# Kernel tuning notes

Measured on AMD Instinct MI355X. Metric: run time of the kernel, lower is better.

The kernel has to match this reference:

```python
import jax, jax.numpy as jnp
import numpy as np

N = 100000          # nodes
E = 1600000         # edges
F = 128             # raw node features
D = 16              # embedding_dim (per-head out channels)
H = 8               # heads
NEG_SLOPE = 0.2     # GATConv leaky_relu slope
EPS = 1e-16         # PyG softmax denominator eps


def _glorot(key, shape):
    fan_in, fan_out = shape[0], shape[-1]
    lim = np.sqrt(6.0 / (fan_in + fan_out))
    return jax.random.uniform(key, shape, jnp.float32, -lim, lim)


def setup_inputs() -> dict:
    key = jax.random.key(0)
    ks = jax.random.split(key, 24)
    x = jax.random.normal(ks[0], (N, F), jnp.float32)
    edge_index = jax.random.randint(ks[1], (2, E), 0, N, jnp.int64)
    HD = H * D
    return {
        "x": x,
        "edge_index": edge_index,
        # attribute embedding Linear(F, D)
        "W_emb": _glorot(ks[2], (F, D)), "b_emb": jnp.zeros((D,), jnp.float32),
        # GAT layer 0: in=D, out=D per head
        "W0": _glorot(ks[3], (D, HD)),
        "as0": _glorot(ks[4], (H, D)), "ad0": _glorot(ks[5], (H, D)),
        "b0": jnp.zeros((HD,), jnp.float32),
        # GAT layer 1: in=H*D, out=D per head
        "W1": _glorot(ks[6], (HD, HD)),
        "as1": _glorot(ks[7], (H, D)), "ad1": _glorot(ks[8], (H, D)),
        "b1": jnp.zeros((HD,), jnp.float32),
        "Wy1": _glorot(ks[9], (HD, 1)), "by1": jnp.zeros((1,), jnp.float32),
        "Wy0": _glorot(ks[10], (HD, 1)), "by0": jnp.zeros((1,), jnp.float32),
        # classifier Linear(HD, D) -> ReLU -> Linear(D, 1) -> Sigmoid
        "Wc1": _glorot(ks[11], (HD, D)), "bc1": jnp.zeros((D,), jnp.float32),
        "Wc2": _glorot(ks[12], (D, 1)), "bc2": jnp.zeros((1,), jnp.float32),
    }


def _gat_conv(h, src, dst, W, att_src, att_dst, bias):
    # h: [N, in] -> out: [N, H*D]; src/dst already include self-loops
    g = (h @ W).reshape(N, H, D)                                   # [N,H,D]
    a_src = jnp.einsum('nhd,hd->nh', g, att_src)                   # [N,H]
    a_dst = jnp.einsum('nhd,hd->nh', g, att_dst)                   # [N,H]
    logits = jax.nn.leaky_relu(a_src[src] + a_dst[dst], NEG_SLOPE) # [Et,H]
    m = jax.ops.segment_max(logits, dst, num_segments=N)           # [N,H]
    ex = jnp.exp(logits - m[dst])
    denom = jax.ops.segment_sum(ex, dst, num_segments=N)           # [N,H]
    alpha = ex / (denom[dst] + EPS)                                # [Et,H]
    msg = g[src] * alpha[..., None]                                # [Et,H,D]
    out = jax.ops.segment_sum(msg, dst, num_segments=N)            # [N,H,D]
    return out.reshape(N, H * D) + bias


def reference(x, edge_index, W_emb, b_emb, W0, as0, ad0, b0,
              W1, as1, ad1, b1, Wy1, by1, Wy0, by0, Wc1, bc1, Wc2, bc2):
    # add self loops (PyG GATConv default)
    loop = jnp.arange(N, dtype=edge_index.dtype)
    src = jnp.concatenate([edge_index[0], loop])
    dst = jnp.concatenate([edge_index[1], loop])

    h = x @ W_emb + b_emb                        # [N,D]
    h = _gat_conv(h, src, dst, W0, as0, ad0, b0) # [N,H*D]
    h = _gat_conv(h, src, dst, W1, as1, ad1, b1) # [N,H*D]

    y1 = h @ Wy1 + by1
    y0 = h @ Wy0 + by0
    causal_effect = y1 - y0                      # [N,1]
    propensity = jax.nn.sigmoid(jax.nn.relu(h @ Wc1 + bc1) @ Wc2 + bc2)  # [N,1]
    return causal_effect, propensity
```

## Files before the change

kernel.cpp:

```cpp
#include <hip/hip_runtime.h>
#include <hip/hip_fp16.h>
#include <math.h>

#define N_NODES 100000
#define E_EDGES 1600000
#define F_IN 128
#define D_DIM 16
#define H_HEADS 8
#define HD 128
#define NEG_SLOPE 0.2f

#define SCAN_BLOCKS 256
#define SCAN_CH ((N_NODES + SCAN_BLOCKS - 1) / SCAN_BLOCKS)

#define NTILES ((N_NODES + 63) / 64)

#define NB_E 196
#define EB 128
#define CH_E ((E_EDGES + EB - 1) / EB)
#define NBB (NB_E * EB)

__global__ __launch_bounds__(256) void embed_kernel(
        const float* __restrict__ x, const float* __restrict__ W,
        const float* __restrict__ b, __half* __restrict__ h0) {
    __shared__ float Ws[F_IN * D_DIM];
    __shared__ float bs[D_DIM];
    __shared__ float xs[16][F_IN + 1];
    int t = threadIdx.x;
    for (int i = t; i < F_IN * D_DIM; i += 256) Ws[i] = W[i];
    if (t < D_DIM) bs[t] = b[t];
    __syncthreads();
    for (int base = blockIdx.x * 16; base < N_NODES; base += gridDim.x * 16) {
        int cnt = min(16, N_NODES - base);
        __syncthreads();
        for (int i = t; i < cnt * F_IN; i += 256) {
            int nn = i >> 7, k = i & 127;
            xs[nn][k] = x[(size_t)(base + nn) * F_IN + k];
        }
        __syncthreads();
        int nn = t >> 4, c = t & 15;
        if (nn < cnt) {
            float a0 = 0.f, a1 = 0.f, a2 = 0.f, a3 = 0.f;
            #pragma unroll
            for (int k = 0; k < F_IN; k += 4) {
                a0 += xs[nn][k + 0] * Ws[(k + 0) * D_DIM + c];
                a1 += xs[nn][k + 1] * Ws[(k + 1) * D_DIM + c];
                a2 += xs[nn][k + 2] * Ws[(k + 2) * D_DIM + c];
                a3 += xs[nn][k + 3] * Ws[(k + 3) * D_DIM + c];
            }
            h0[(size_t)(base + nn) * D_DIM + c] =
                __float2half((a0 + a1) + (a2 + a3) + bs[c]);
        }
    }
}

__global__ __launch_bounds__(256) void precompute_kernel(
        const float* __restrict__ W0, const float* __restrict__ W1,
        const float* __restrict__ as0, const float* __restrict__ ad0,
        const float* __restrict__ b0,
        float* __restrict__ W_fused, float* __restrict__ u_s,
        float* __restrict__ u_d, float* __restrict__ bvec) {
    int t = threadIdx.x;
    if (t < 128) {
        int h = t >> 4, c = t & 15;
        float ss = 0.f, sd = 0.f;
        for (int dp = 0; dp < 16; ++dp) {
            float w = W0[c * HD + h * 16 + dp];
            ss += w * as0[h * 16 + dp];
            sd += w * ad0[h * 16 + dp];
        }
        u_s[t] = ss; u_d[t] = sd;
        float bb = 0.f;
        for (int k = 0; k < HD; ++k) bb += b0[k] * W1[k * HD + t];
        bvec[t] = bb;
    }
    for (int idx = t; idx < HD * HD; idx += 256) {
        int i = idx >> 7, j = idx & 127;
        int h = i >> 4, c = i & 15;
        float s = 0.f;
        for (int dp = 0; dp < 16; ++dp)
            s += W0[c * HD + h * 16 + dp] * W1[(h * 16 + dp) * HD + j];
        W_fused[idx] = s;
    }
}

__global__ __launch_bounds__(256) void attdot0_kernel(
        const __half* __restrict__ h0, const float* __restrict__ u_s,
        const float* __restrict__ u_d,
        float* __restrict__ a_s, float* __restrict__ a_d) {
    __shared__ float us[128], ud[128];
    int t = threadIdx.x;
    if (t < 128) { us[t] = u_s[t]; ud[t] = u_d[t]; }
    __syncthreads();
    int gidx = blockIdx.x * 256 + t;
    int n = gidx >> 3, h = gidx & 7;
    if (n >= N_NODES) return;
    const __half2* hp = (const __half2*)(h0 + (size_t)n * D_DIM);
    float ss = 0.f, sd = 0.f;
    #pragma unroll
    for (int c2 = 0; c2 < 8; ++c2) {
        float2 f = __half22float2(hp[c2]);
        ss += f.x * us[h * 16 + 2 * c2] + f.y * us[h * 16 + 2 * c2 + 1];
        sd += f.x * ud[h * 16 + 2 * c2] + f.y * ud[h * 16 + 2 * c2 + 1];
    }
    a_s[n * 8 + h] = ss;
    a_d[n * 8 + h] = sd;
}

__global__ __launch_bounds__(256) void transform_fused_kernel(
        const __half* __restrict__ m, const float* __restrict__ W,
        const float* __restrict__ bvec,
        const float* __restrict__ att_s, const float* __restrict__ att_d,
        __half* __restrict__ g, float* __restrict__ a_src, float* __restrict__ a_dst) {
    __shared__ float Ws[128][64];
    __shared__ float hs[64][128 + 4];
    int t = threadIdx.x;
    int cq = t & 15;
    int nq = t >> 4;

    for (int item = blockIdx.x; item < NTILES * 2; item += gridDim.x) {
        int tile = item >> 1;
        int coff = (item & 1) << 6;
        int nbase = tile << 6;
        __syncthreads();
        for (int i = t; i < 128 * 64; i += 256)
            Ws[i >> 6][i & 63] = W[(size_t)(i >> 6) * HD + coff + (i & 63)];
        for (int i = t; i < (128 << 6); i += 256) {
            int r = i >> 7, k = i & 127;
            int n = nbase + r; if (n >= N_NODES) n = N_NODES - 1;
            hs[r][k] = __half2float(m[(size_t)n * HD + k]);
        }
        __syncthreads();

        float acc[4][4] = {{0.f}};
        #pragma unroll 2
        for (int k = 0; k < 128; k += 4) {
            float4 w0 = *(const float4*)&Ws[k + 0][cq << 2];
            float4 w1 = *(const float4*)&Ws[k + 1][cq << 2];
            float4 w2 = *(const float4*)&Ws[k + 2][cq << 2];
            float4 w3 = *(const float4*)&Ws[k + 3][cq << 2];
            #pragma unroll
            for (int j = 0; j < 4; ++j) {
                float4 hv = *(const float4*)&hs[(nq << 2) + j][k];
                acc[j][0] += hv.x * w0.x + hv.y * w1.x + hv.z * w2.x + hv.w * w3.x;
                acc[j][1] += hv.x * w0.y + hv.y * w1.y + hv.z * w2.y + hv.w * w3.y;
                acc[j][2] += hv.x * w0.z + hv.y * w1.z + hv.z * w2.z + hv.w * w3.z;
                acc[j][3] += hv.x * w0.w + hv.y * w1.w + hv.z * w2.w + hv.w * w3.w;
            }
        }

        int c0 = coff + (cq << 2);
        float bq0 = bvec[c0], bq1 = bvec[c0 + 1], bq2 = bvec[c0 + 2], bq3 = bvec[c0 + 3];
        float as0 = att_s[c0], as1 = att_s[c0 + 1], as2 = att_s[c0 + 2], as3 = att_s[c0 + 3];
        float ad0 = att_d[c0], ad1 = att_d[c0 + 1], ad2 = att_d[c0 + 2], ad3 = att_d[c0 + 3];
        int head = c0 >> 4;
        #pragma unroll
        for (int j = 0; j < 4; ++j) {
            int n = nbase + (nq << 2) + j;
            float g0 = acc[j][0] + bq0, g1v = acc[j][1] + bq1;
            float g2 = acc[j][2] + bq2, g3v = acc[j][3] + bq3;
            float ps = g0 * as0 + g1v * as1 + g2 * as2 + g3v * as3;
            float pd = g0 * ad0 + g1v * ad1 + g2 * ad2 + g3v * ad3;
            ps += __shfl_xor(ps, 1); ps += __shfl_xor(ps, 2);
            pd += __shfl_xor(pd, 1); pd += __shfl_xor(pd, 2);
            if (n < N_NODES) {
                union { __half2 h2[2]; uint2 u; } pk;
                pk.h2[0] = __floats2half2_rn(g0, g1v);
                pk.h2[1] = __floats2half2_rn(g2, g3v);
                *(uint2*)&g[(size_t)n * HD + c0] = pk.u;
                if ((cq & 3) == 0) {
                    a_src[(size_t)n * H_HEADS + head] = ps;
                    a_dst[(size_t)n * H_HEADS + head] = pd;
                }
            }
        }
    }
}

__global__ __launch_bounds__(256) void epart_count_kernel(
        const int* __restrict__ ei, int* __restrict__ bcountE) {
    __shared__ int lh[NB_E];
    int b = blockIdx.x, t = threadIdx.x;
    int lo = b * CH_E, hi = min(lo + CH_E, E_EDGES);
    for (int i = t; i < NB_E; i += 256) lh[i] = 0;
    __syncthreads();
    for (int e = lo + t; e < hi; e += 256)
        atomicAdd(&lh[ei[E_EDGES + e] >> 9], 1);
    __syncthreads();
    for (int i = t; i < NB_E; i += 256) bcountE[i * EB + b] = lh[i];
}

__global__ __launch_bounds__(1024) void escan_kernel(
        const int* __restrict__ bcountE, int* __restrict__ ebaseBB) {
    __shared__ int part[1024];
    int t = threadIdx.x;
    int lo = t * 25, hi = min(lo + 25, NBB);
    int s = 0;
    for (int i = lo; i < hi; ++i) s += bcountE[i];
    part[t] = s;
    __syncthreads();
    int val = s;
    for (int off = 1; off < 1024; off <<= 1) {
        int o = (t >= off) ? part[t - off] : 0;
        __syncthreads();
        val += o;
        part[t] = val;
        __syncthreads();
    }
    int run = val - s;
    for (int i = lo; i < hi; ++i) { ebaseBB[i] = run; run += bcountE[i]; }
}

__global__ __launch_bounds__(256) void epart_write_kernel(
        const int* __restrict__ ei, const int* __restrict__ ebaseBB,
        int* __restrict__ epack) {
    __shared__ int lbase[NB_E];
    int b = blockIdx.x, t = threadIdx.x;
    int lo = b * CH_E, hi = min(lo + CH_E, E_EDGES);
    for (int i = t; i < NB_E; i += 256) lbase[i] = ebaseBB[i * EB + b];
    __syncthreads();
    for (int e = lo + t; e < hi; e += 256) {
        int s = ei[e], d = ei[E_EDGES + e];
        int p = atomicAdd(&lbase[d >> 9], 1);
        epack[p] = (s << 9) | (d & 511);
    }
}

__global__ __launch_bounds__(256) void bucket_build_kernel(
        const int* __restrict__ ebaseBB, const int* __restrict__ epack,
        int* __restrict__ row_ptr, int* __restrict__ col) {
    __shared__ int lh[512];
    __shared__ int sc[256];
    __shared__ int lfill[512];
    int b = blockIdx.x, t = threadIdx.x;
    int lo = ebaseBB[b * EB];
    int hi = (b == NB_E - 1) ? E_EDGES : ebaseBB[(b + 1) * EB];
    lh[t] = 0; lh[t + 256] = 0;
    __syncthreads();
    for (int i = lo + t; i < hi; i += 256)
        atomicAdd(&lh[epack[i] & 511], 1);
    __syncthreads();
    int c0 = lh[2 * t], c1 = lh[2 * t + 1];
    int pairSum = c0 + c1;
    sc[t] = pairSum;
    __syncthreads();
    int val = pairSum;
    for (int off = 1; off < 256; off <<= 1) {
        int o = (t >= off) ? sc[t - off] : 0;
        __syncthreads();
        val += o;
        sc[t] = val;
        __syncthreads();
    }
    int excl2 = val - pairSum;
    int p0 = lo + excl2, p1 = lo + excl2 + c0;
    lfill[2 * t] = p0;
    lfill[2 * t + 1] = p1;
    int nb0 = b * 512;
    if (nb0 + 2 * t     <= N_NODES) row_ptr[nb0 + 2 * t]     = p0;
    if (nb0 + 2 * t + 1 <= N_NODES) row_ptr[nb0 + 2 * t + 1] = p1;
    __syncthreads();
    for (int i = lo + t; i < hi; i += 256) {
        int v = epack[i];
        int p = atomicAdd(&lfill[v & 511], 1);
        col[p] = ((unsigned)v) >> 9;
    }
}

__global__ __launch_bounds__(256) void bucket_hist_kernel(
        const int* __restrict__ row_ptr, int* __restrict__ bcount) {
    __shared__ int lh[64];
    int b = blockIdx.x, t = threadIdx.x;
    if (t < 64) lh[t] = 0;
    __syncthreads();
    int lo = b * SCAN_CH, hi = min(lo + SCAN_CH, N_NODES);
    for (int i = lo + t; i < hi; i += 256) {
        int dg = row_ptr[i + 1] - row_ptr[i];
        atomicAdd(&lh[min(dg, 63)], 1);
    }
    __syncthreads();
    if (t < 64) bcount[t * SCAN_BLOCKS + b] = lh[t];
}

__global__ __launch_bounds__(1024) void bucket_scan_kernel(
        const int* __restrict__ bcount, int* __restrict__ boffs) {
    __shared__ int part[1024];
    int t = threadIdx.x;
    int base = t * 16;
    int v[16]; int s = 0;
    #pragma unroll
    for (int k = 0; k < 16; ++k) { v[k] = bcount[base + k]; s += v[k]; }
    part[t] = s;
    __syncthreads();
    int val = s;
    for (int off = 1; off < 1024; off <<= 1) {
        int o = (t >= off) ? part[t - off] : 0;
        __syncthreads();
        val += o;
        part[t] = val;
        __syncthreads();
    }
    int run = val - s;
    #pragma unroll
    for (int k = 0; k < 16; ++k) { boffs[base + k] = run; run += v[k]; }
}

__global__ __launch_bounds__(256) void bucket_scatter_kernel(
        const int* __restrict__ row_ptr, const int* __restrict__ boffs,
        int* __restrict__ perm) {
    __shared__ int lbase[64];
    int b = blockIdx.x, t = threadIdx.x;
    if (t < 64) lbase[t] = boffs[t * SCAN_BLOCKS + b];
    __syncthreads();
    int lo = b * SCAN_CH, hi = min(lo + SCAN_CH, N_NODES);
    for (int i = lo + t; i < hi; i += 256) {
        int dg = row_ptr[i + 1] - row_ptr[i];
        int p = atomicAdd(&lbase[min(dg, 63)], 1);
        perm[p] = i;
    }
}

__global__ __launch_bounds__(256) void gat_aggr0_kernel(
        const int* __restrict__ perm,
        const int* __restrict__ row_ptr, const int* __restrict__ col,
        const float* __restrict__ a_src, const float* __restrict__ a_dst,
        const __half* __restrict__ h0, __half* __restrict__ m) {
    int wv = threadIdx.x >> 6, lane = threadIdx.x & 63;
    int grp = lane >> 4;
    int sub = lane & 15;
    int cq = sub & 3;
    int hp = sub >> 2;
    int slot = blockIdx.x * 16 + wv * 4 + grp;
    bool dvalid = slot < N_NODES;
    int d = perm[dvalid ? slot : N_NODES - 1];

    int i0 = row_ptr[d], end = row_ptr[d + 1];
    int deg = dvalid ? (end - i0) : 0;
    float2 ad = *(const float2*)(a_dst + (size_t)d * 8 + 2 * hp);

    float acc0[4], acc1[4];
    float den0, den1;
    {
        float2 as = *(const float2*)(a_src + (size_t)d * 8 + 2 * hp);
        float l0 = as.x + ad.x; l0 = fmaxf(l0, NEG_SLOPE * l0);
        float l1 = as.y + ad.y; l1 = fmaxf(l1, NEG_SLOPE * l1);
        float w0 = __expf(l0), w1 = __expf(l1);
        uint2 hv = *(const uint2*)(h0 + (size_t)d * D_DIM + 4 * cq);
        float2 fa = __half22float2(*(__half2*)&hv.x);
        float2 fb = __half22float2(*(__half2*)&hv.y);
        acc0[0] = w0 * fa.x; acc0[1] = w0 * fa.y;
        acc0[2] = w0 * fb.x; acc0[3] = w0 * fb.y;
        acc1[0] = w1 * fa.x; acc1[1] = w1 * fa.y;
        acc1[2] = w1 * fb.x; acc1[3] = w1 * fb.y;
        den0 = w0; den1 = w1;
    }

    int md = deg;
    md = max(md, __shfl_xor(md, 16));
    md = max(md, __shfl_xor(md, 32));

    int colv = 0;
    #define EDGE_K(EL)                                                       \
    {                                                                        \
        int el_ = (EL);                                                      \
        int s = __shfl(colv, (grp << 4) | (el_ & 15));                       \
        float2 as = *(const float2*)(a_src + (size_t)s * 8 + 2 * hp);        \
        float l0 = as.x + ad.x; l0 = fmaxf(l0, NEG_SLOPE * l0);              \
        float l1 = as.y + ad.y; l1 = fmaxf(l1, NEG_SLOPE * l1);              \
        float w0 = (el_ < deg) ? __expf(l0) : 0.f;                           \
        float w1 = (el_ < deg) ? __expf(l1) : 0.f;                           \
        uint2 hv = *(const uint2*)(h0 + (size_t)s * D_DIM + 4 * cq);         \
        float2 fa = __half22float2(*(__half2*)&hv.x);                        \
        float2 fb = __half22float2(*(__half2*)&hv.y);                        \
        acc0[0] += w0 * fa.x; acc0[1] += w0 * fa.y;                          \
        acc0[2] += w0 * fb.x; acc0[3] += w0 * fb.y;                          \
        acc1[0] += w1 * fa.x; acc1[1] += w1 * fa.y;                          \
        acc1[2] += w1 * fb.x; acc1[3] += w1 * fb.y;                          \
        den0 += w0; den1 += w1;                                              \
    }

    for (int el = 0; el < md; el += 4) {
        if ((el & 15) == 0) {
            int ci = i0 + el + sub;
            ci = min(ci, end - 1);
            ci = max(ci, 0);
            colv = col[ci];
        }
        EDGE_K(el);
        EDGE_K(el + 1);
        EDGE_K(el + 2);
        EDGE_K(el + 3);
    }
    #undef EDGE_K

    float inv0 = 1.f / (den0 + 1e-16f);
    float inv1 = 1.f / (den1 + 1e-16f);
    if (dvalid) {
        union { __half2 h2[2]; uint2 u; } p0, p1;
        p0.h2[0] = __floats2half2_rn(acc0[0] * inv0, acc0[1] * inv0);
        p0.h2[1] = __floats2half2_rn(acc0[2] * inv0, acc0[3] * inv0);
        p1.h2[0] = __floats2half2_rn(acc1[0] * inv1, acc1[1] * inv1);
        p1.h2[1] = __floats2half2_rn(acc1[2] * inv1, acc1[3] * inv1);
        *(uint2*)(m + (size_t)d * HD + (2 * hp) * 16 + 4 * cq)       = p0.u;
        *(uint2*)(m + (size_t)d * HD + (2 * hp + 1) * 16 + 4 * cq)   = p1.u;
    }
}

__global__ __launch_bounds__(256) void gat_aggr1_kernel(
        const int* __restrict__ perm,
        const int* __restrict__ row_ptr, const int* __restrict__ col,
        const float* __restrict__ a_src, const float* __restrict__ a_dst,
        const __half* __restrict__ g, const float* __restrict__ bias,
        float* __restrict__ out,
        const float* __restrict__ Wy1, const float* __restrict__ by1,
        const float* __restrict__ Wy0, const float* __restrict__ by0,
        const float* __restrict__ Wc1, const float* __restrict__ bc1,
        const float* __restrict__ Wc2, const float* __restrict__ bc2) {
    int wv = threadIdx.x >> 6, lane = threadIdx.x & 63;
    int grp = lane >> 4;
    int sub = lane & 15;
    int hh  = sub >> 1;
    int slot = blockIdx.x * 16 + wv * 4 + grp;
    bool dvalid = slot < N_NODES;
    int d = perm[dvalid ? slot : N_NODES - 1];

    int i0 = row_ptr[d], end = row_ptr[d + 1];
    int deg = dvalid ? (end - i0) : 0;
    float ad = a_dst[d * 8 + hh];

    float acc[8];
    float den;
    {
        float a = a_src[d * 8 + hh] + ad;
        a = fmaxf(a, NEG_SLOPE * a);
        float w = __expf(a);
        uint4 rv = *(const uint4*)(g + (size_t)d * HD + (sub << 3));
        float2 f0 = __half22float2(*(__half2*)&rv.x);
        float2 f1 = __half22float2(*(__half2*)&rv.y);
        float2 f2 = __half22float2(*(__half2*)&rv.z);
        float2 f3 = __half22float2(*(__half2*)&rv.w);
        acc[0] = w * f0.x; acc[1] = w * f0.y;
        acc[2] = w * f1.x; acc[3] = w * f1.y;
        acc[4] = w * f2.x; acc[5] = w * f2.y;
        acc[6] = w * f3.x; acc[7] = w * f3.y;
        den = w;
    }

    int md = deg;
    md = max(md, __shfl_xor(md, 16));
    md = max(md, __shfl_xor(md, 32));

    int colv = 0;
    #define EDGE_K(EL)                                                       \
    {                                                                        \
        int el_ = (EL);                                                      \
        int s = __shfl(colv, (grp << 4) | (el_ & 15));                       \
        float a = a_src[s * 8 + hh] + ad;                                    \
        a = fmaxf(a, NEG_SLOPE * a);                                         \
        float w = (el_ < deg) ? __expf(a) : 0.f;                             \
        uint4 rv = *(const uint4*)(g + (size_t)s * HD + (sub << 3));         \
        float2 f0 = __half22float2(*(__half2*)&rv.x);                        \
        float2 f1 = __half22float2(*(__half2*)&rv.y);                        \
        float2 f2 = __half22float2(*(__half2*)&rv.z);                        \
        float2 f3 = __half22float2(*(__half2*)&rv.w);                        \
        acc[0] += w * f0.x; acc[1] += w * f0.y;                              \
        acc[2] += w * f1.x; acc[3] += w * f1.y;                              \
        acc[4] += w * f2.x; acc[5] += w * f2.y;                              \
        acc[6] += w * f3.x; acc[7] += w * f3.y;                              \
        den += w;                                                            \
    }

    for (int el = 0; el < md; el += 4) {
        if ((el & 15) == 0) {
            int ci = i0 + el + sub;
            ci = min(ci, end - 1);
            ci = max(ci, 0);
            colv = col[ci];
        }
        EDGE_K(el);
        EDGE_K(el + 1);
        EDGE_K(el + 2);
        EDGE_K(el + 3);
    }
    #undef EDGE_K

    float inv = 1.f / (den + 1e-16f);
    int c0 = sub << 3;
    float h[8];
    #pragma unroll
    for (int k = 0; k < 8; ++k) h[k] = acc[k] * inv + bias[c0 + k];

    float p = 0.f;
    #pragma unroll
    for (int k = 0; k < 8; ++k)
        p += h[k] * (Wy1[c0 + k] - Wy0[c0 + k]);
    p += __shfl_xor(p, 1); p += __shfl_xor(p, 2);
    p += __shfl_xor(p, 4); p += __shfl_xor(p, 8);
    float acc2 = 0.f;
    #pragma unroll
    for (int j = 0; j < D_DIM; ++j) {
        float q = 0.f;
        #pragma unroll
        for (int k = 0; k < 8; ++k)
            q += h[k] * Wc1[(c0 + k) * D_DIM + j];
        q += __shfl_xor(q, 1); q += __shfl_xor(q, 2);
        q += __shfl_xor(q, 4); q += __shfl_xor(q, 8);
        float z = q + bc1[j];
        z = (z > 0.f) ? z : 0.f;
        acc2 += z * Wc2[j];
    }
    if (sub == 0 && dvalid) {
        out[d] = p + by1[0] - by0[0];
        out[N_NODES + d] = 1.f / (1.f + __expf(-(acc2 + bc2[0])));
    }
}

extern "C" void kernel_launch(void* const* d_in, const int* in_sizes, int n_in,
                              void* d_out, int out_size, void* d_ws, size_t ws_size,
                              hipStream_t stream) {
    const float* x     = (const float*)d_in[0];
    const int*   ei    = (const int*)  d_in[1];
    const float* W_emb = (const float*)d_in[2];
    const float* b_emb = (const float*)d_in[3];
    const float* W0    = (const float*)d_in[4];
    const float* as0   = (const float*)d_in[5];
    const float* ad0   = (const float*)d_in[6];
    const float* b0    = (const float*)d_in[7];
    const float* W1    = (const float*)d_in[8];
    const float* as1   = (const float*)d_in[9];
    const float* ad1   = (const float*)d_in[10];
    const float* b1    = (const float*)d_in[11];
    const float* Wy1   = (const float*)d_in[12];
    const float* by1   = (const float*)d_in[13];
    const float* Wy0   = (const float*)d_in[14];
    const float* by0   = (const float*)d_in[15];
    const float* Wc1   = (const float*)d_in[16];
    const float* bc1   = (const float*)d_in[17];
    const float* Wc2   = (const float*)d_in[18];
    const float* bc2   = (const float*)d_in[19];
    float* out = (float*)d_out;

    float* ws    = (float*)d_ws;
    __half* mH   = (__half*)ws;
    __half* gH   = (__half*)(ws + (size_t)N_NODES * 64);
    __half* h0h  = (__half*)(ws + (size_t)N_NODES * 128);
    float* a_s   = ws + (size_t)N_NODES * 136;
    float* a_d   = a_s + (size_t)N_NODES * 8;
    float* Wf    = a_d + (size_t)N_NODES * 8;
    float* u_s   = Wf + 16384;
    float* u_d   = u_s + 128;
    float* bvec  = u_d + 128;
    int*   row_ptr = (int*)(bvec + 128);
    int*   bcountE = row_ptr + (N_NODES + 1);
    int*   ebaseBB = bcountE + NBB;
    int*   bcount  = ebaseBB + NBB;
    int*   boffs   = bcount + 64 * SCAN_BLOCKS;
    int*   perm    = boffs + 64 * SCAN_BLOCKS;
    int*   col     = perm + N_NODES;
    int*   epack   = col + E_EDGES;

    int aggrBlocks = (N_NODES + 15) / 16;

    hipLaunchKernelGGL(epart_count_kernel, dim3(EB), dim3(256), 0, stream,
                       ei, bcountE);
    hipLaunchKernelGGL(escan_kernel, dim3(1), dim3(1024), 0, stream,
                       bcountE, ebaseBB);
    hipLaunchKernelGGL(epart_write_kernel, dim3(EB), dim3(256), 0, stream,
                       ei, ebaseBB, epack);
    hipLaunchKernelGGL(bucket_build_kernel, dim3(NB_E), dim3(256), 0, stream,
                       ebaseBB, epack, row_ptr, col);

    hipLaunchKernelGGL(bucket_hist_kernel, dim3(SCAN_BLOCKS), dim3(256), 0, stream,
                       row_ptr, bcount);
    hipLaunchKernelGGL(bucket_scan_kernel, dim3(1), dim3(1024), 0, stream,
                       bcount, boffs);
    hipLaunchKernelGGL(bucket_scatter_kernel, dim3(SCAN_BLOCKS), dim3(256), 0, stream,
                       row_ptr, boffs, perm);

    hipLaunchKernelGGL(embed_kernel, dim3(512), dim3(256), 0, stream,
                       x, W_emb, b_emb, h0h);
    hipLaunchKernelGGL(precompute_kernel, dim3(1), dim3(256), 0, stream,
                       W0, W1, as0, ad0, b0, Wf, u_s, u_d, bvec);

    hipLaunchKernelGGL(attdot0_kernel, dim3((N_NODES * 8 + 255) / 256), dim3(256),
                       0, stream, h0h, u_s, u_d, a_s, a_d);
    hipLaunchKernelGGL(gat_aggr0_kernel, dim3(aggrBlocks), dim3(256), 0, stream,
                       perm, row_ptr, col, a_s, a_d, h0h, mH);

    hipLaunchKernelGGL(transform_fused_kernel, dim3(1024), dim3(256), 0, stream,
                       mH, Wf, bvec, as1, ad1, gH, a_s, a_d);
    hipLaunchKernelGGL(gat_aggr1_kernel, dim3(aggrBlocks), dim3(256), 0, stream,
                       perm, row_ptr, col, a_s, a_d, gH, b1, out,
                       Wy1, by1, Wy0, by0, Wc1, bc1, Wc2, bc2);
}
```

Baseline: 415.9 us.

## Fuse attention dots into embed, degree histogram into bucket build, half smem tiles

Layer-0 attention-score computation moves into the embedding kernel through shuffle reductions, so the separate attdot kernel and its re-read of h0 go away. The degree histogram is now built inside bucket_build per 512-node bucket, which removes the bucket_hist kernel, and the scatter is regridded to match. transform_fused keeps its node tile in shared memory as half with vectorised uint4 loads, halving shared-memory footprint and converting on read. The aggregation loops are unrolled by 8 instead of 4. Embed drops its bounds check, which relies on N being a multiple of 16.

```diff
diff --git a/kernel.cpp b/kernel.cpp
--- a/kernel.cpp
+++ b/kernel.cpp
@@ -10,46 +10,58 @@
 #define HD 128
 #define NEG_SLOPE 0.2f
 
-#define SCAN_BLOCKS 256
-#define SCAN_CH ((N_NODES + SCAN_BLOCKS - 1) / SCAN_BLOCKS)
-
 #define NTILES ((N_NODES + 63) / 64)
 
 #define NB_E 196
 #define EB 128
 #define CH_E ((E_EDGES + EB - 1) / EB)
 #define NBB (NB_E * EB)
+#define NDB (64 * NB_E)
 
 __global__ __launch_bounds__(256) void embed_kernel(
         const float* __restrict__ x, const float* __restrict__ W,
-        const float* __restrict__ b, __half* __restrict__ h0) {
+        const float* __restrict__ b, const float* __restrict__ u_s,
+        const float* __restrict__ u_d,
+        __half* __restrict__ h0, float* __restrict__ a_s,
+        float* __restrict__ a_d) {
     __shared__ float Ws[F_IN * D_DIM];
     __shared__ float bs[D_DIM];
+    __shared__ float us[128], ud[128];
     __shared__ float xs[16][F_IN + 1];
     int t = threadIdx.x;
     for (int i = t; i < F_IN * D_DIM; i += 256) Ws[i] = W[i];
     if (t < D_DIM) bs[t] = b[t];
+    if (t >= 64 && t < 192) { us[t - 64] = u_s[t - 64]; ud[t - 64] = u_d[t - 64]; }
     __syncthreads();
     for (int base = blockIdx.x * 16; base < N_NODES; base += gridDim.x * 16) {
-        int cnt = min(16, N_NODES - base);
-        __syncthreads();
-        for (int i = t; i < cnt * F_IN; i += 256) {
+        __syncthreads();
+        for (int i = t; i < 16 * F_IN; i += 256) {
             int nn = i >> 7, k = i & 127;
             xs[nn][k] = x[(size_t)(base + nn) * F_IN + k];
         }
         __syncthreads();
         int nn = t >> 4, c = t & 15;
-        if (nn < cnt) {
-            float a0 = 0.f, a1 = 0.f, a2 = 0.f, a3 = 0.f;
-            #pragma unroll
-            for (int k = 0; k < F_IN; k += 4) {
-                a0 += xs[nn][k + 0] * Ws[(k + 0) * D_DIM + c];
-                a1 += xs[nn][k + 1] * Ws[(k + 1) * D_DIM + c];
-                a2 += xs[nn][k + 2] * Ws[(k + 2) * D_DIM + c];
-                a3 += xs[nn][k + 3] * Ws[(k + 3) * D_DIM + c];
-            }
-            h0[(size_t)(base + nn) * D_DIM + c] =
-                __float2half((a0 + a1) + (a2 + a3) + bs[c]);
+        int n = base + nn;
+        float a0 = 0.f, a1 = 0.f, a2 = 0.f, a3 = 0.f;
+        #pragma unroll
+        for (int k = 0; k < F_IN; k += 4) {
+            a0 += xs[nn][k + 0] * Ws[(k + 0) * D_DIM + c];
+            a1 += xs[nn][k + 1] * Ws[(k + 1) * D_DIM + c];
+            a2 += xs[nn][k + 2] * Ws[(k + 2) * D_DIM + c];
+            a3 += xs[nn][k + 3] * Ws[(k + 3) * D_DIM + c];
+        }
+        float hv = (a0 + a1) + (a2 + a3) + bs[c];
+        h0[(size_t)n * D_DIM + c] = __float2half(hv);
+        #pragma unroll
+        for (int h = 0; h < 8; ++h) {
+            float ps = hv * us[h * 16 + c];
+            float pd = hv * ud[h * 16 + c];
+            ps += __shfl_xor(ps, 1); ps += __shfl_xor(ps, 2);
+            ps += __shfl_xor(ps, 4); ps += __shfl_xor(ps, 8);
+            pd += __shfl_xor(pd, 1); pd += __shfl_xor(pd, 2);
+            pd += __shfl_xor(pd, 4); pd += __shfl_xor(pd, 8);
+            if (c == h)     a_s[(size_t)n * 8 + h] = ps;
+            if (c == h + 8) a_d[(size_t)n * 8 + h] = pd;
         }
     }
 }
@@ -84,36 +96,13 @@
     }
 }
 
-__global__ __launch_bounds__(256) void attdot0_kernel(
-        const __half* __restrict__ h0, const float* __restrict__ u_s,
-        const float* __restrict__ u_d,
-        float* __restrict__ a_s, float* __restrict__ a_d) {
-    __shared__ float us[128], ud[128];
-    int t = threadIdx.x;
-    if (t < 128) { us[t] = u_s[t]; ud[t] = u_d[t]; }
-    __syncthreads();
-    int gidx = blockIdx.x * 256 + t;
-    int n = gidx >> 3, h = gidx & 7;
-    if (n >= N_NODES) return;
-    const __half2* hp = (const __half2*)(h0 + (size_t)n * D_DIM);
-    float ss = 0.f, sd = 0.f;
-    #pragma unroll
-    for (int c2 = 0; c2 < 8; ++c2) {
-        float2 f = __half22float2(hp[c2]);
-        ss += f.x * us[h * 16 + 2 * c2] + f.y * us[h * 16 + 2 * c2 + 1];
-        sd += f.x * ud[h * 16 + 2 * c2] + f.y * ud[h * 16 + 2 * c2 + 1];
-    }
-    a_s[n * 8 + h] = ss;
-    a_d[n * 8 + h] = sd;
-}
-
 __global__ __launch_bounds__(256) void transform_fused_kernel(
         const __half* __restrict__ m, const float* __restrict__ W,
         const float* __restrict__ bvec,
         const float* __restrict__ att_s, const float* __restrict__ att_d,
         __half* __restrict__ g, float* __restrict__ a_src, float* __restrict__ a_dst) {
     __shared__ float Ws[128][64];
-    __shared__ float hs[64][128 + 4];
+    __shared__ __half hs[64][136];
     int t = threadIdx.x;
     int cq = t & 15;
     int nq = t >> 4;
@@ -125,10 +114,10 @@
         __syncthreads();
         for (int i = t; i < 128 * 64; i += 256)
             Ws[i >> 6][i & 63] = W[(size_t)(i >> 6) * HD + coff + (i & 63)];
-        for (int i = t; i < (128 << 6); i += 256) {
-            int r = i >> 7, k = i & 127;
+        for (int i = t; i < 64 * 16; i += 256) {
+            int r = i >> 4, k8 = (i & 15) << 3;
             int n = nbase + r; if (n >= N_NODES) n = N_NODES - 1;
-            hs[r][k] = __half2float(m[(size_t)n * HD + k]);
+            *(uint4*)&hs[r][k8] = *(const uint4*)(m + (size_t)n * HD + k8);
         }
         __syncthreads();
 
@@ -141,11 +130,13 @@
             float4 w3 = *(const float4*)&Ws[k + 3][cq << 2];
             #pragma unroll
             for (int j = 0; j < 4; ++j) {
-                float4 hv = *(const float4*)&hs[(nq << 2) + j][k];
-                acc[j][0] += hv.x * w0.x + hv.y * w1.x + hv.z * w2.x + hv.w * w3.x;
-                acc[j][1] += hv.x * w0.y + hv.y * w1.y + hv.z * w2.y + hv.w * w3.y;
-                acc[j][2] += hv.x * w0.z + hv.y * w1.z + hv.z * w2.z + hv.w * w3.z;
-                acc[j][3] += hv.x * w0.w + hv.y * w1.w + hv.z * w2.w + hv.w * w3.w;
+                uint2 hv2 = *(const uint2*)&hs[(nq << 2) + j][k];
+                float2 fa = __half22float2(*(__half2*)&hv2.x);
+                float2 fb = __half22float2(*(__half2*)&hv2.y);
+                acc[j][0] += fa.x * w0.x + fa.y * w1.x + fb.x * w2.x + fb.y * w3.x;
+                acc[j][1] += fa.x * w0.y + fa.y * w1.y + fb.x * w2.y + fb.y * w3.y;
+                acc[j][2] += fa.x * w0.z + fa.y * w1.z + fb.x * w2.z + fb.y * w3.z;
+                acc[j][3] += fa.x * w0.w + fa.y * w1.w + fb.x * w2.w + fb.y * w3.w;
             }
         }
 
@@ -228,14 +219,17 @@
 
 __global__ __launch_bounds__(256) void bucket_build_kernel(
         const int* __restrict__ ebaseBB, const int* __restrict__ epack,
-        int* __restrict__ row_ptr, int* __restrict__ col) {
+        int* __restrict__ row_ptr, int* __restrict__ col,
+        int* __restrict__ bcount) {
     __shared__ int lh[512];
     __shared__ int sc[256];
     __shared__ int lfill[512];
+    __shared__ int dh[64];
     int b = blockIdx.x, t = threadIdx.x;
     int lo = ebaseBB[b * EB];
     int hi = (b == NB_E - 1) ? E_EDGES : ebaseBB[(b + 1) * EB];
     lh[t] = 0; lh[t + 256] = 0;
+    if (t < 64) dh[t] = 0;
     __syncthreads();
     for (int i = lo + t; i < hi; i += 256)
         atomicAdd(&lh[epack[i] & 511], 1);
@@ -259,37 +253,24 @@
     int nb0 = b * 512;
     if (nb0 + 2 * t     <= N_NODES) row_ptr[nb0 + 2 * t]     = p0;
     if (nb0 + 2 * t + 1 <= N_NODES) row_ptr[nb0 + 2 * t + 1] = p1;
+    if (nb0 + 2 * t     < N_NODES) atomicAdd(&dh[min(c0, 63)], 1);
+    if (nb0 + 2 * t + 1 < N_NODES) atomicAdd(&dh[min(c1, 63)], 1);
     __syncthreads();
     for (int i = lo + t; i < hi; i += 256) {
         int v = epack[i];
         int p = atomicAdd(&lfill[v & 511], 1);
         col[p] = ((unsigned)v) >> 9;
     }
-}
-
-__global__ __launch_bounds__(256) void bucket_hist_kernel(
-        const int* __restrict__ row_ptr, int* __restrict__ bcount) {
-    __shared__ int lh[64];
-    int b = blockIdx.x, t = threadIdx.x;
-    if (t < 64) lh[t] = 0;
-    __syncthreads();
-    int lo = b * SCAN_CH, hi = min(lo + SCAN_CH, N_NODES);
-    for (int i = lo + t; i < hi; i += 256) {
-        int dg = row_ptr[i + 1] - row_ptr[i];
-        atomicAdd(&lh[min(dg, 63)], 1);
-    }
-    __syncthreads();
-    if (t < 64) bcount[t * SCAN_BLOCKS + b] = lh[t];
+    if (t < 64) bcount[t * NB_E + b] = dh[t];
 }
 
 __global__ __launch_bounds__(1024) void bucket_scan_kernel(
         const int* __restrict__ bcount, int* __restrict__ boffs) {
     __shared__ int part[1024];
     int t = threadIdx.x;
-    int base = t * 16;
-    int v[16]; int s = 0;
-    #pragma unroll
-    for (int k = 0; k < 16; ++k) { v[k] = bcount[base + k]; s += v[k]; }
+    int lo = t * 13, hi = min(lo + 13, NDB);
+    int s = 0;
+    for (int i = lo; i < hi; ++i) s += bcount[i];
     part[t] = s;
     __syncthreads();
     int val = s;
@@ -301,8 +282,7 @@
         __syncthreads();
     }
     int run = val - s;
-    #pragma unroll
-    for (int k = 0; k < 16; ++k) { boffs[base + k] = run; run += v[k]; }
+    for (int i = lo; i < hi; ++i) { boffs[i] = run; run += bcount[i]; }
 }
 
 __global__ __launch_bounds__(256) void bucket_scatter_kernel(
@@ -310,13 +290,16 @@
         int* __restrict__ perm) {
     __shared__ int lbase[64];
     int b = blockIdx.x, t = threadIdx.x;
-    if (t < 64) lbase[t] = boffs[t * SCAN_BLOCKS + b];
-    __syncthreads();
-    int lo = b * SCAN_CH, hi = min(lo + SCAN_CH, N_NODES);
-    for (int i = lo + t; i < hi; i += 256) {
-        int dg = row_ptr[i + 1] - row_ptr[i];
-        int p = atomicAdd(&lbase[min(dg, 63)], 1);
-        perm[p] = i;
+    if (t < 64) lbase[t] = boffs[t * NB_E + b];
+    __syncthreads();
+    int nb0 = b * 512;
+    for (int k = t; k < 512; k += 256) {
+        int i = nb0 + k;
+        if (i < N_NODES) {
+            int dg = row_ptr[i + 1] - row_ptr[i];
+            int p = atomicAdd(&lbase[min(dg, 63)], 1);
+            perm[p] = i;
+        }
     }
 }
 
@@ -379,17 +362,17 @@
         den0 += w0; den1 += w1;                                              \
     }
 
-    for (int el = 0; el < md; el += 4) {
+    for (int el = 0; el < md; el += 8) {
         if ((el & 15) == 0) {
             int ci = i0 + el + sub;
             ci = min(ci, end - 1);
             ci = max(ci, 0);
             colv = col[ci];
         }
-        EDGE_K(el);
-        EDGE_K(el + 1);
-        EDGE_K(el + 2);
-        EDGE_K(el + 3);
+        EDGE_K(el);     EDGE_K(el + 1);
+        EDGE_K(el + 2); EDGE_K(el + 3);
+        EDGE_K(el + 4); EDGE_K(el + 5);
+        EDGE_K(el + 6); EDGE_K(el + 7);
     }
     #undef EDGE_K
 
@@ -470,17 +453,17 @@
         den += w;                                                            \
     }
 
-    for (int el = 0; el < md; el += 4) {
+    for (int el = 0; el < md; el += 8) {
         if ((el & 15) == 0) {
             int ci = i0 + el + sub;
             ci = min(ci, end - 1);
             ci = max(ci, 0);
             colv = col[ci];
         }
-        EDGE_K(el);
-        EDGE_K(el + 1);
-        EDGE_K(el + 2);
-        EDGE_K(el + 3);
+        EDGE_K(el);     EDGE_K(el + 1);
+        EDGE_K(el + 2); EDGE_K(el + 3);
+        EDGE_K(el + 4); EDGE_K(el + 5);
+        EDGE_K(el + 6); EDGE_K(el + 7);
     }
     #undef EDGE_K
 
@@ -554,8 +537,8 @@
     int*   bcountE = row_ptr + (N_NODES + 1);
     int*   ebaseBB = bcountE + NBB;
     int*   bcount  = ebaseBB + NBB;
-    int*   boffs   = bcount + 64 * SCAN_BLOCKS;
-    int*   perm    = boffs + 64 * SCAN_BLOCKS;
+    int*   boffs   = bcount + NDB;
+    int*   perm    = boffs + NDB;
     int*   col     = perm + N_NODES;
     int*   epack   = col + E_EDGES;
 
@@ -568,22 +551,18 @@
     hipLaunchKernelGGL(epart_write_kernel, dim3(EB), dim3(256), 0, stream,
                        ei, ebaseBB, epack);
     hipLaunchKernelGGL(bucket_build_kernel, dim3(NB_E), dim3(256), 0, stream,
-                       ebaseBB, epack, row_ptr, col);
-
-    hipLaunchKernelGGL(bucket_hist_kernel, dim3(SCAN_BLOCKS), dim3(256), 0, stream,
-                       row_ptr, bcount);
+                       ebaseBB, epack, row_ptr, col, bcount);
+
     hipLaunchKernelGGL(bucket_scan_kernel, dim3(1), dim3(1024), 0, stream,
                        bcount, boffs);
-    hipLaunchKernelGGL(bucket_scatter_kernel, dim3(SCAN_BLOCKS), dim3(256), 0, stream,
+    hipLaunchKernelGGL(bucket_scatter_kernel, dim3(NB_E), dim3(256), 0, stream,
                        row_ptr, boffs, perm);
 
-    hipLaunchKernelGGL(embed_kernel, dim3(512), dim3(256), 0, stream,
-                       x, W_emb, b_emb, h0h);
     hipLaunchKernelGGL(precompute_kernel, dim3(1), dim3(256), 0, stream,
                        W0, W1, as0, ad0, b0, Wf, u_s, u_d, bvec);
-
-    hipLaunchKernelGGL(attdot0_kernel, dim3((N_NODES * 8 + 255) / 256), dim3(256),
-                       0, stream, h0h, u_s, u_d, a_s, a_d);
+    hipLaunchKernelGGL(embed_kernel, dim3(512), dim3(256), 0, stream,
+                       x, W_emb, b_emb, u_s, u_d, h0h, a_s, a_d);
+
     hipLaunchKernelGGL(gat_aggr0_kernel, dim3(aggrBlocks), dim3(256), 0, stream,
                        perm, row_ptr, col, a_s, a_d, h0h, mH);
 
```

Result: slower. 426.9 us (+2.6%).
